# Kernel optimization log

Measured on AMD Instinct MI355X. Metric: run time of the kernel, lower is better.

Reference implementation:

```python
import jax, jax.numpy as jnp
import numpy as np

H, W, C_IN, C_OUT, B = 256, 256, 64, 64, 2
NEG_SLOPE = 0.2


def make_grid_edges(h, w, b):
    """8-neighborhood grid edges + self-loops (GATConv add_self_loops), batched with node offsets."""
    idx = np.arange(h * w).reshape(h, w)
    src_l, dst_l = [], []
    for dr in (-1, 0, 1):
        for dc in (-1, 0, 1):
            rs = slice(max(0, -dr), h - max(0, dr))
            cs = slice(max(0, -dc), w - max(0, dc))
            dst = idx[rs, cs]
            src = idx[rs.start + dr:rs.stop + dr, cs.start + dc:cs.stop + dc]
            src_l.append(src.ravel())
            dst_l.append(dst.ravel())
    s = np.concatenate(src_l)
    d = np.concatenate(dst_l)
    offs = (np.arange(b) * h * w)[:, None]
    return (s[None] + offs).ravel().astype(np.int32), (d[None] + offs).ravel().astype(np.int32)


def setup_inputs() -> dict:
    key = jax.random.key(0)
    ks = jax.random.split(key, 7)
    x = jax.random.normal(ks[0], (B, C_IN, H, W), dtype=jnp.float32)
    pos_w = jax.random.normal(ks[1], (2, C_IN), dtype=jnp.float32) * (1.0 / np.sqrt(2.0))
    pos_b = jax.random.normal(ks[2], (C_IN,), dtype=jnp.float32) * 0.1
    lin_w = jax.random.normal(ks[3], (C_IN, C_OUT), dtype=jnp.float32) * (1.0 / np.sqrt(C_IN))
    att_src = jax.random.normal(ks[4], (C_OUT,), dtype=jnp.float32) * (1.0 / np.sqrt(C_OUT))
    att_dst = jax.random.normal(ks[5], (C_OUT,), dtype=jnp.float32) * (1.0 / np.sqrt(C_OUT))
    bias = jax.random.normal(ks[6], (C_OUT,), dtype=jnp.float32) * 0.1
    es, ed = make_grid_edges(H, W, B)
    return {"x": x, "pos_w": pos_w, "pos_b": pos_b, "lin_w": lin_w,
            "att_src": att_src, "att_dst": att_dst, "bias": bias,
            "edge_src": jnp.asarray(es), "edge_dst": jnp.asarray(ed)}


def reference(x, pos_w, pos_b, lin_w, att_src, att_dst, bias, edge_src, edge_dst):
    b, c, h, w = x.shape
    n = h * w
    num_nodes = b * n
    # positional encoding: pos[h,w] = (y, x) in [-1,1]
    px = jnp.linspace(-1.0, 1.0, w)
    py = jnp.linspace(-1.0, 1.0, h)
    gx, gy = jnp.meshgrid(px, py, indexing="xy")          # (H, W)
    pos = jnp.stack([gy, gx], axis=-1)                     # (H, W, 2)
    pe = pos @ pos_w + pos_b                               # (H, W, C)
    xg = (x + pe.transpose(2, 0, 1)[None]).transpose(0, 2, 3, 1).reshape(num_nodes, c)
    # GATConv, heads=1: linear transform, per-edge attention logits
    hfeat = xg @ lin_w                                     # (BN, Cout)
    a_src = hfeat @ att_src                                # (BN,)
    a_dst = hfeat @ att_dst                                # (BN,)
    e = jax.nn.leaky_relu(a_src[edge_src] + a_dst[edge_dst], NEG_SLOPE)  # (E,)
    # segment softmax over incoming edges of each target node
    m = jax.ops.segment_max(e, edge_dst, num_segments=num_nodes)
    p = jnp.exp(e - m[edge_dst])
    s = jax.ops.segment_sum(p, edge_dst, num_segments=num_nodes)
    alpha = p / s[edge_dst]                                # (E,)
    # scatter-add aggregation of weighted messages
    out = jax.ops.segment_sum(alpha[:, None] * hfeat[edge_src], edge_dst,
                              num_segments=num_nodes) + bias
    return out.reshape(b, h, w, -1).transpose(0, 3, 1, 2)
```

## Files before the change

### kernel.cpp

```cpp
#include <hip/hip_runtime.h>

#define HGT 256
#define WID 256
#define CH  64
#define NB  2
#define HW  (HGT * WID)
#define NODES (NB * HW)
#define NEG_SLOPE 0.2f

typedef float f32x16 __attribute__((ext_vector_type(16)));
typedef short short8 __attribute__((ext_vector_type(8)));

__device__ __forceinline__ unsigned short f2bf(float f) {
    union { float f; unsigned u; } v; v.f = f;
    unsigned r = v.u + 0x7FFF + ((v.u >> 16) & 1);
    return (unsigned short)(r >> 16);
}

__global__ __launch_bounds__(512) void gat_feat(
    const float* __restrict__ x, const float* __restrict__ pos_w,
    const float* __restrict__ pos_b, const float* __restrict__ lin_w,
    const float* __restrict__ att_src, const float* __restrict__ att_dst,
    unsigned short* __restrict__ hfeat, float* __restrict__ asrc,
    float* __restrict__ adst)
{
    __shared__ __align__(16) unsigned char wlds[CH * 128];
    __shared__ __align__(16) float W0s[CH], W1s[CH], Bcs[CH], atts[CH], attd[CH];

    const int tid  = threadIdx.x;
    const int lane = tid & 63;
    const int wid  = tid >> 6;
    const int hi   = lane >> 5;
    const int col  = lane & 31;

    {
        const int co  = tid & 63;
        const int cib = (tid >> 6) * 8;
        unsigned char* rowp = wlds + co * 128;
        const unsigned sw = (unsigned)((co & 7) << 4);
        #pragma unroll
        for (int p = 0; p < 4; ++p) {
            const int ci = cib + 2 * p;
            const unsigned lo = f2bf(lin_w[ci * CH + co]);
            const unsigned hh = f2bf(lin_w[(ci + 1) * CH + co]);
            *(unsigned*)(rowp + (((unsigned)(2 * ci)) ^ sw)) = lo | (hh << 16);
        }
    }
    if (tid < CH) {
        float w0 = 0.f, w1 = 0.f, bc = 0.f;
        for (int ci = 0; ci < CH; ++ci) {
            const float lwv = lin_w[ci * CH + tid];
            w0 = fmaf(pos_w[ci],      lwv, w0);
            w1 = fmaf(pos_w[CH + ci], lwv, w1);
            bc = fmaf(pos_b[ci],      lwv, bc);
        }
        W0s[tid] = w0; W1s[tid] = w1; Bcs[tid] = bc;
    } else if (tid < 128) {
        atts[tid - 64] = att_src[tid - 64];
    } else if (tid < 192) {
        attd[tid - 128] = att_dst[tid - 128];
    }
    __syncthreads();

    short8 a0[4], a1[4];
    {
        const unsigned sw = (unsigned)((col & 7) << 4);
        #pragma unroll
        for (int ks = 0; ks < 4; ++ks) {
            const unsigned off = (unsigned)(32 * ks + 16 * hi) ^ sw;
            a0[ks] = *(const short8*)(wlds + col * 128 + off);
            a1[ks] = *(const short8*)(wlds + (32 + col) * 128 + off);
        }
    }

    const int g     = blockIdx.x * 8 + wid;
    const int node0 = g * 32;
    const int b     = node0 >> 16;
    const int hw    = (node0 & (HW - 1)) + col;
    const int node  = node0 + col;

    const float* xp = x + (size_t)b * CH * HW + hw;
    float xv[32];
    #pragma unroll
    for (int ks = 0; ks < 4; ++ks)
        #pragma unroll
        for (int e = 0; e < 8; ++e)
            xv[ks * 8 + e] = xp[(size_t)(16 * ks + 8 * hi + e) * HW];

    short8 bk[4];
    #pragma unroll
    for (int ks = 0; ks < 4; ++ks)
        #pragma unroll
        for (int e = 0; e < 8; ++e)
            bk[ks][e] = (short)f2bf(xv[ks * 8 + e]);

    f32x16 acc0, acc1;
    #pragma unroll
    for (int k = 0; k < 16; ++k) { acc0[k] = 0.f; acc1[k] = 0.f; }

    #pragma unroll
    for (int ks = 0; ks < 4; ++ks) {
        acc0 = __builtin_amdgcn_mfma_f32_32x32x16_bf16(a0[ks], bk[ks], acc0, 0, 0, 0);
        acc1 = __builtin_amdgcn_mfma_f32_32x32x16_bf16(a1[ks], bk[ks], acc1, 0, 0, 0);
    }

    const int ii = hw >> 8, jj = hw & 255;
    const float py = -1.f + (2.f / 255.f) * (float)ii;
    const float px = -1.f + (2.f / 255.f) * (float)jj;

    uint2* hq = (uint2*)hfeat + (size_t)b * 16 * HW + hw;
    float as = 0.f, ad = 0.f;

    #pragma unroll
    for (int t = 0; t < 2; ++t) {
        const f32x16 A = (t == 0) ? acc0 : acc1;
        #pragma unroll
        for (int q2 = 0; q2 < 4; ++q2) {
            const int cb = 32 * t + 8 * q2 + 4 * hi;
            const float4 w0 = *(const float4*)&W0s[cb];
            const float4 w1 = *(const float4*)&W1s[cb];
            const float4 bc = *(const float4*)&Bcs[cb];
            const float4 s4 = *(const float4*)&atts[cb];
            const float4 d4 = *(const float4*)&attd[cb];
            const float h0 = A[4 * q2 + 0] + py * w0.x + px * w1.x + bc.x;
            const float h1 = A[4 * q2 + 1] + py * w0.y + px * w1.y + bc.y;
            const float h2 = A[4 * q2 + 2] + py * w0.z + px * w1.z + bc.z;
            const float h3 = A[4 * q2 + 3] + py * w0.w + px * w1.w + bc.w;
            as += h0 * s4.x + h1 * s4.y + h2 * s4.z + h3 * s4.w;
            ad += h0 * d4.x + h1 * d4.y + h2 * d4.z + h3 * d4.w;
            const unsigned u0 = (unsigned)f2bf(h0) | ((unsigned)f2bf(h1) << 16);
            const unsigned u1 = (unsigned)f2bf(h2) | ((unsigned)f2bf(h3) << 16);
            const int q = 8 * t + 2 * q2 + hi;
            hq[(size_t)q * HW] = make_uint2(u0, u1);
        }
    }

    as += __shfl_xor(as, 32);
    ad += __shfl_xor(ad, 32);
    if (hi == 0) { asrc[node] = as; adst[node] = ad; }
}

__global__ __launch_bounds__(256) void gat_aggr(
    const unsigned short* __restrict__ hfeat, const float* __restrict__ asrc,
    const float* __restrict__ adst, const float* __restrict__ bias,
    float* __restrict__ out)
{
    const int tid = threadIdx.x;
    const int tx  = tid & 63;
    const int ty  = tid >> 6;

    const int raw = blockIdx.x;
    const int wg  = (raw & 7) * 1024 + (raw >> 3);
    const int qg    = wg & 3;
    const int chunk = (wg >> 2) & 3;
    const int bi    = wg >> 4;
    const int i     = bi & (HGT - 1);
    const int b     = bi >> 8;
    const int j     = chunk * 64 + tx;
    const int hw    = i * WID + j;
    const int node  = b * HW + hw;
    const int q     = __builtin_amdgcn_readfirstlane(qg * 4 + ty);

    const float adv = adst[node];

    float w[9];
    int   off[9];
    float m = -1e30f;
    #pragma unroll
    for (int t = 0; t < 9; ++t) {
        const int dr = t / 3 - 1, dc = t % 3 - 1;
        const int r = i + dr, c = j + dc;
        const bool ok = (r >= 0) && (r < HGT) && (c >= 0) && (c < WID);
        off[t] = ok ? (dr * WID + dc) : 0;
        float ev = -1e30f;
        if (ok) {
            ev = asrc[node + off[t]] + adv;
            ev = (ev >= 0.f) ? ev : NEG_SLOPE * ev;
        }
        w[t] = ev;
        m = fmaxf(m, ev);
    }

    float s = 0.f;
    #pragma unroll
    for (int t = 0; t < 9; ++t) {
        const float p = (w[t] > -1e29f) ? __expf(w[t] - m) : 0.f;
        w[t] = p; s += p;
    }
    const float inv = 1.f / s;

    const uint2* hq = (const uint2*)hfeat + (size_t)(b * 16 + q) * HW + hw;

    float a0 = 0.f, a1 = 0.f, a2 = 0.f, a3 = 0.f;
    #pragma unroll
    for (int t = 0; t < 9; ++t) {
        const uint2 v  = hq[off[t]];
        const float wt = w[t] * inv;
        a0 = fmaf(wt, __uint_as_float(v.x << 16),         a0);
        a1 = fmaf(wt, __uint_as_float(v.x & 0xffff0000u), a1);
        a2 = fmaf(wt, __uint_as_float(v.y << 16),         a2);
        a3 = fmaf(wt, __uint_as_float(v.y & 0xffff0000u), a3);
    }

    float* ob = out + (size_t)(b * CH + q * 4) * HW + hw;
    ob[0 * (size_t)HW] = a0 + bias[q * 4 + 0];
    ob[1 * (size_t)HW] = a1 + bias[q * 4 + 1];
    ob[2 * (size_t)HW] = a2 + bias[q * 4 + 2];
    ob[3 * (size_t)HW] = a3 + bias[q * 4 + 3];
}

extern "C" void kernel_launch(void* const* d_in, const int* in_sizes, int n_in,
                              void* d_out, int out_size, void* d_ws, size_t ws_size,
                              hipStream_t stream) {
    const float* x       = (const float*)d_in[0];
    const float* pos_w   = (const float*)d_in[1];
    const float* pos_b   = (const float*)d_in[2];
    const float* lin_w   = (const float*)d_in[3];
    const float* att_src = (const float*)d_in[4];
    const float* att_dst = (const float*)d_in[5];
    const float* bias    = (const float*)d_in[6];

    float* out = (float*)d_out;
    unsigned short* hfeat = (unsigned short*)d_ws;
    float* asrc = (float*)((char*)d_ws + (size_t)NODES * CH * 2);
    float* adst = asrc + NODES;

    gat_feat<<<dim3(512), dim3(512), 0, stream>>>(
        x, pos_w, pos_b, lin_w, att_src, att_dst, hfeat, asrc, adst);
    gat_aggr<<<dim3(8192), dim3(256), 0, stream>>>(
        hfeat, asrc, adst, bias, out);
}
```

Before: 125.9 us.

## Hoist weight preprocessing into a single-block prep kernel, shrink feature blocks

Moves the per-block bf16 conversion of lin_w and the positional-encoding weight folding out of gat_feat into a separate one-block gat_prep kernel that writes them to workspace. gat_feat then loads A fragments and the folded vectors straight from global memory (cached), with no LDS staging or __syncthreads, and runs as 1024 blocks of 256 threads. The aim is to stop every block from redoing the 64-iteration serial reduction and weight conversion. In exchange it adds a kernel launch plus a dependency between kernels, and gat_feat now reads its weights from global/L2 instead of LDS.

Result: no change. 127.2 us (+1.0%).

```diff
diff --git a/kernel.cpp b/kernel.cpp
--- a/kernel.cpp
+++ b/kernel.cpp
@@ -17,68 +17,78 @@
     return (unsigned short)(r >> 16);
 }
 
-__global__ __launch_bounds__(512) void gat_feat(
-    const float* __restrict__ x, const float* __restrict__ pos_w,
-    const float* __restrict__ pos_b, const float* __restrict__ lin_w,
-    const float* __restrict__ att_src, const float* __restrict__ att_dst,
+__global__ __launch_bounds__(256) void gat_prep(
+    const float* __restrict__ lin_w, const float* __restrict__ pos_w,
+    const float* __restrict__ pos_b,
+    float* __restrict__ W0, float* __restrict__ W1, float* __restrict__ Bc,
+    unsigned short* __restrict__ wt)
+{
+    __shared__ float r0[4][64], r1[4][64], r2[4][64];
+    const int tid = threadIdx.x;
+    const int co  = tid & 63;
+    const int ty  = tid >> 6;
+
+    float w0 = 0.f, w1 = 0.f, bc = 0.f;
+    #pragma unroll
+    for (int p = 0; p < 16; ++p) {
+        const int ci = ty * 16 + p;
+        const float lwv = lin_w[ci * CH + co];
+        w0 = fmaf(pos_w[ci],      lwv, w0);
+        w1 = fmaf(pos_w[CH + ci], lwv, w1);
+        bc = fmaf(pos_b[ci],      lwv, bc);
+    }
+    r0[ty][co] = w0; r1[ty][co] = w1; r2[ty][co] = bc;
+
+    {
+        const int pco = tid >> 2;
+        const int cib = (tid & 3) * 16;
+        unsigned u[8];
+        #pragma unroll
+        for (int e = 0; e < 16; e += 2) {
+            const unsigned lo = f2bf(lin_w[(cib + e)     * CH + pco]);
+            const unsigned hh = f2bf(lin_w[(cib + e + 1) * CH + pco]);
+            u[e >> 1] = lo | (hh << 16);
+        }
+        uint4* dst = (uint4*)(wt + pco * CH + cib);
+        dst[0] = make_uint4(u[0], u[1], u[2], u[3]);
+        dst[1] = make_uint4(u[4], u[5], u[6], u[7]);
+    }
+
+    __syncthreads();
+    if (ty == 0) {
+        W0[co] = r0[0][co] + r0[1][co] + r0[2][co] + r0[3][co];
+        W1[co] = r1[0][co] + r1[1][co] + r1[2][co] + r1[3][co];
+        Bc[co] = r2[0][co] + r2[1][co] + r2[2][co] + r2[3][co];
+    }
+}
+
+__global__ __launch_bounds__(256, 3) void gat_feat(
+    const float* __restrict__ x, const float* __restrict__ att_src,
+    const float* __restrict__ att_dst, const float* __restrict__ W0s,
+    const float* __restrict__ W1s, const float* __restrict__ Bcs,
+    const unsigned short* __restrict__ wt,
     unsigned short* __restrict__ hfeat, float* __restrict__ asrc,
     float* __restrict__ adst)
 {
-    __shared__ __align__(16) unsigned char wlds[CH * 128];
-    __shared__ __align__(16) float W0s[CH], W1s[CH], Bcs[CH], atts[CH], attd[CH];
-
     const int tid  = threadIdx.x;
     const int lane = tid & 63;
     const int wid  = tid >> 6;
     const int hi   = lane >> 5;
     const int col  = lane & 31;
 
-    {
-        const int co  = tid & 63;
-        const int cib = (tid >> 6) * 8;
-        unsigned char* rowp = wlds + co * 128;
-        const unsigned sw = (unsigned)((co & 7) << 4);
-        #pragma unroll
-        for (int p = 0; p < 4; ++p) {
-            const int ci = cib + 2 * p;
-            const unsigned lo = f2bf(lin_w[ci * CH + co]);
-            const unsigned hh = f2bf(lin_w[(ci + 1) * CH + co]);
-            *(unsigned*)(rowp + (((unsigned)(2 * ci)) ^ sw)) = lo | (hh << 16);
-        }
-    }
-    if (tid < CH) {
-        float w0 = 0.f, w1 = 0.f, bc = 0.f;
-        for (int ci = 0; ci < CH; ++ci) {
-            const float lwv = lin_w[ci * CH + tid];
-            w0 = fmaf(pos_w[ci],      lwv, w0);
-            w1 = fmaf(pos_w[CH + ci], lwv, w1);
-            bc = fmaf(pos_b[ci],      lwv, bc);
-        }
-        W0s[tid] = w0; W1s[tid] = w1; Bcs[tid] = bc;
-    } else if (tid < 128) {
-        atts[tid - 64] = att_src[tid - 64];
-    } else if (tid < 192) {
-        attd[tid - 128] = att_dst[tid - 128];
-    }
-    __syncthreads();
-
-    short8 a0[4], a1[4];
-    {
-        const unsigned sw = (unsigned)((col & 7) << 4);
-        #pragma unroll
-        for (int ks = 0; ks < 4; ++ks) {
-            const unsigned off = (unsigned)(32 * ks + 16 * hi) ^ sw;
-            a0[ks] = *(const short8*)(wlds + col * 128 + off);
-            a1[ks] = *(const short8*)(wlds + (32 + col) * 128 + off);
-        }
-    }
-
-    const int g     = blockIdx.x * 8 + wid;
+    const int g     = blockIdx.x * 4 + wid;
     const int node0 = g * 32;
     const int b     = node0 >> 16;
     const int hw    = (node0 & (HW - 1)) + col;
     const int node  = node0 + col;
 
+    short8 a0[4], a1[4];
+    #pragma unroll
+    for (int ks = 0; ks < 4; ++ks) {
+        a0[ks] = *(const short8*)(wt + col * CH        + ks * 16 + hi * 8);
+        a1[ks] = *(const short8*)(wt + (32 + col) * CH + ks * 16 + hi * 8);
+    }
+
     const float* xp = x + (size_t)b * CH * HW + hw;
     float xv[32];
     #pragma unroll
@@ -87,21 +97,18 @@
         for (int e = 0; e < 8; ++e)
             xv[ks * 8 + e] = xp[(size_t)(16 * ks + 8 * hi + e) * HW];
 
-    short8 bk[4];
-    #pragma unroll
-    for (int ks = 0; ks < 4; ++ks)
+    f32x16 acc0, acc1;
+    #pragma unroll
+    for (int k = 0; k < 16; ++k) { acc0[k] = 0.f; acc1[k] = 0.f; }
+
+    #pragma unroll
+    for (int ks = 0; ks < 4; ++ks) {
+        short8 bk;
         #pragma unroll
         for (int e = 0; e < 8; ++e)
-            bk[ks][e] = (short)f2bf(xv[ks * 8 + e]);
-
-    f32x16 acc0, acc1;
-    #pragma unroll
-    for (int k = 0; k < 16; ++k) { acc0[k] = 0.f; acc1[k] = 0.f; }
-
-    #pragma unroll
-    for (int ks = 0; ks < 4; ++ks) {
-        acc0 = __builtin_amdgcn_mfma_f32_32x32x16_bf16(a0[ks], bk[ks], acc0, 0, 0, 0);
-        acc1 = __builtin_amdgcn_mfma_f32_32x32x16_bf16(a1[ks], bk[ks], acc1, 0, 0, 0);
+            bk[e] = (short)f2bf(xv[ks * 8 + e]);
+        acc0 = __builtin_amdgcn_mfma_f32_32x32x16_bf16(a0[ks], bk, acc0, 0, 0, 0);
+        acc1 = __builtin_amdgcn_mfma_f32_32x32x16_bf16(a1[ks], bk, acc1, 0, 0, 0);
     }
 
     const int ii = hw >> 8, jj = hw & 255;
@@ -120,8 +127,8 @@
             const float4 w0 = *(const float4*)&W0s[cb];
             const float4 w1 = *(const float4*)&W1s[cb];
             const float4 bc = *(const float4*)&Bcs[cb];
-            const float4 s4 = *(const float4*)&atts[cb];
-            const float4 d4 = *(const float4*)&attd[cb];
+            const float4 s4 = *(const float4*)&att_src[cb];
+            const float4 d4 = *(const float4*)&att_dst[cb];
             const float h0 = A[4 * q2 + 0] + py * w0.x + px * w1.x + bc.x;
             const float h1 = A[4 * q2 + 1] + py * w0.y + px * w1.y + bc.y;
             const float h2 = A[4 * q2 + 2] + py * w0.z + px * w1.z + bc.z;
@@ -221,12 +228,18 @@
     const float* bias    = (const float*)d_in[6];
 
     float* out = (float*)d_out;
-    unsigned short* hfeat = (unsigned short*)d_ws;
-    float* asrc = (float*)((char*)d_ws + (size_t)NODES * CH * 2);
+    char*  ws  = (char*)d_ws;
+    unsigned short* hfeat = (unsigned short*)ws;
+    float* asrc = (float*)(ws + (size_t)NODES * CH * 2);
     float* adst = asrc + NODES;
-
-    gat_feat<<<dim3(512), dim3(512), 0, stream>>>(
-        x, pos_w, pos_b, lin_w, att_src, att_dst, hfeat, asrc, adst);
+    float* W0   = adst + NODES;
+    float* W1   = W0 + CH;
+    float* Bc   = W1 + CH;
+    unsigned short* wt = (unsigned short*)(Bc + CH);
+
+    gat_prep<<<dim3(1), dim3(256), 0, stream>>>(lin_w, pos_w, pos_b, W0, W1, Bc, wt);
+    gat_feat<<<dim3(1024), dim3(256), 0, stream>>>(
+        x, att_src, att_dst, W0, W1, Bc, wt, hfeat, asrc, adst);
     gat_aggr<<<dim3(8192), dim3(256), 0, stream>>>(
         hfeat, asrc, adst, bias, out);
 }
```
